# Kernel optimization log

Measured on AMD Instinct MI355X. Metric: run time of the kernel, lower is better.

## Reference

```python
import jax, jax.numpy as jnp
import numpy as np

N = 8192   # number of nodes
C = 16     # number of classes / clusters


def setup_inputs() -> dict:
    key = jax.random.key(0)
    k1, k2 = jax.random.split(key)
    H_i = jax.random.normal(k1, (N, C), dtype=jnp.float32)
    A_i = jax.random.normal(k2, (N, N), dtype=jnp.float32)
    return {"H_i": H_i, "A_i": A_i}


def reference(H_i, A_i):
    # adj = (A_i > 0), boolean adjacency (non-differentiable threshold)
    adj = (A_i > 0).astype(H_i.dtype)          # [N, N]
    deg = jnp.sum(adj, axis=0)                 # [N] node degrees
    s = jnp.sum(adj)                           # scalar: total edge weight (2m)
    # trace(H^T B H) with B = adj - outer(deg, deg)/s, computed without
    # materializing B:  trace(H^T adj H) = sum(H * (adj @ H)),
    # trace(H^T outer(deg,deg) H) = (deg @ H) . (deg @ H)
    quad = jnp.sum(H_i * (adj @ H_i))          # sum_c h_c^T adj h_c
    dH = deg @ H_i                             # [C]
    loss = (quad - jnp.dot(dH, dH) / s) / s
    return loss
```

## Files before the change

### kernel.cpp

```cpp
#include <hip/hip_runtime.h>
#include <hip/hip_bf16.h>
#include <stdint.h>

#define NN 8192
#define CC 16
#define RPB 64
#define COLSPLIT 16
#define CPB (NN / COLSPLIT)
#define NCHUNK (NN / 32)
#define ITERS (CPB / 32)
#define NBLK ((NN / RPB) * COLSPLIT)

typedef __attribute__((ext_vector_type(8))) short bf16x8;
typedef __attribute__((ext_vector_type(4))) float f32x4;
typedef __attribute__((ext_vector_type(4))) unsigned int u32x4;


__device__ __forceinline__ unsigned short f32_to_bf16(float f) {
  unsigned int u = __float_as_uint(f);
  u = u + 0x7FFFu + ((u >> 16) & 1u);
  return (unsigned short)(u >> 16);
}
__device__ __forceinline__ float bf16_to_f32(unsigned short h) {
  return __uint_as_float(((unsigned int)h) << 16);
}

__global__ void prep_btab(const float* __restrict__ H, u32x4* __restrict__ btab) {
  int t = blockIdx.x * blockDim.x + threadIdx.x;
  int lane = t & 63;
  int chunk = (t >> 6) & (NCHUNK - 1);
  int pass = t >> 14;
  int c = lane & 15, q = lane >> 4;
  int j0 = chunk * 32 + q * 8;
  unsigned int w[4];
#pragma unroll
  for (int p = 0; p < 4; ++p) {
    unsigned int r = 0;
#pragma unroll
    for (int e = 0; e < 2; ++e) {
      float x = H[(size_t)(j0 + 2 * p + e) * CC + c];
      unsigned short hb = f32_to_bf16(x);
      unsigned short bits = hb;
      if (pass) bits = f32_to_bf16(x - bf16_to_f32(hb));
      r |= ((unsigned int)bits) << (16 * e);
    }
    w[p] = r;
  }
  u32x4 o; o.x = w[0]; o.y = w[1]; o.z = w[2]; o.w = w[3];
  btab[t] = o;
}

__global__ __launch_bounds__(256, 4) void main_k(
    const float* __restrict__ A, const float* __restrict__ H,
    const u32x4* __restrict__ btab,
    double* __restrict__ quad_p, int* __restrict__ cnt_p,
    double* __restrict__ dh_p) {
  __shared__ float sdH[4][16];
  __shared__ float squad[4];
  __shared__ int scnt[4];

  int tid = threadIdx.x;
  int wave = tid >> 6, lane = tid & 63;
  int rb = blockIdx.x / COLSPLIT, cb = blockIdx.x % COLSPLIT;
  int m = lane & 15, q = lane >> 4;
  int row0 = rb * RPB + wave * 16;
  int col0 = cb * CPB;

  const float* arow = A + (size_t)(row0 + m) * NN + col0 + q * 8;
  int chunk0 = col0 >> 5;
  const u32x4* bth = btab + (size_t)chunk0 * 64 + lane;
  const u32x4* btl = bth + (size_t)NCHUNK * 64;

  f32x4 acc_h = {0.f, 0.f, 0.f, 0.f};
  f32x4 acc_l = {0.f, 0.f, 0.f, 0.f};
  int cnt = 0;

#pragma unroll 2
  for (int it = 0; it < ITERS; ++it) {
    f32x4 a0 = *(const f32x4*)(arow + it * 32);
    f32x4 a1 = *(const f32x4*)(arow + it * 32 + 4);
    u32x4 bh = bth[it * 64];
    u32x4 bl = btl[it * 64];
    unsigned int p0 = (a0.x > 0.f ? 0x3F80u : 0u) | (a0.y > 0.f ? 0x3F800000u : 0u);
    unsigned int p1 = (a0.z > 0.f ? 0x3F80u : 0u) | (a0.w > 0.f ? 0x3F800000u : 0u);
    unsigned int p2 = (a1.x > 0.f ? 0x3F80u : 0u) | (a1.y > 0.f ? 0x3F800000u : 0u);
    unsigned int p3 = (a1.z > 0.f ? 0x3F80u : 0u) | (a1.w > 0.f ? 0x3F800000u : 0u);
    cnt += __popc(p0 & 0x00800080u) + __popc(p1 & 0x00800080u) +
           __popc(p2 & 0x00800080u) + __popc(p3 & 0x00800080u);
    u32x4 af; af.x = p0; af.y = p1; af.z = p2; af.w = p3;
    bf16x8 afrag = __builtin_bit_cast(bf16x8, af);
    acc_h = __builtin_amdgcn_mfma_f32_16x16x32_bf16(afrag, __builtin_bit_cast(bf16x8, bh), acc_h, 0, 0, 0);
    acc_l = __builtin_amdgcn_mfma_f32_16x16x32_bf16(afrag, __builtin_bit_cast(bf16x8, bl), acc_l, 0, 0, 0);
  }

  f32x4 af = acc_h + acc_l;

  float rowsum = af.x + af.y + af.z + af.w;
  rowsum += __shfl_xor(rowsum, 16, 64);
  rowsum += __shfl_xor(rowsum, 32, 64);

  const float* hr = H + (size_t)(row0 + q * 4) * CC + m;
  float qp = af.x * hr[0] + af.y * hr[CC] + af.z * hr[2 * CC] + af.w * hr[3 * CC];
#pragma unroll
  for (int d = 1; d < 64; d <<= 1) qp += __shfl_xor(qp, d, 64);
#pragma unroll
  for (int d = 1; d < 64; d <<= 1) cnt += __shfl_xor(cnt, d, 64);

  if (lane < 16) sdH[wave][lane] = rowsum;
  if (lane == 0) { squad[wave] = qp; scnt[wave] = cnt; }
  __syncthreads();
  int bid = blockIdx.x;
  if (tid < 16) {
    dh_p[(size_t)bid * 16 + tid] =
        (double)(sdH[0][tid] + sdH[1][tid] + sdH[2][tid] + sdH[3][tid]);
  } else if (tid == 16) {
    quad_p[bid] = (double)(squad[0] + squad[1] + squad[2] + squad[3]);
  } else if (tid == 17) {
    cnt_p[bid] = scnt[0] + scnt[1] + scnt[2] + scnt[3];
  }
}

__global__ __launch_bounds__(256) void reduce_finalize(
    const double* __restrict__ quad_p, const int* __restrict__ cnt_p,
    const double* __restrict__ dh_p, float* __restrict__ out) {
  __shared__ double sq[4];
  __shared__ long long sc[4];
  __shared__ double sdh[4][16];
  int t = threadIdx.x;
  int wave = t >> 6, lane = t & 63;

  double q = 0.0;
  long long c = 0;
  double dh[16];
#pragma unroll
  for (int k = 0; k < 16; ++k) dh[k] = 0.0;

  for (int b = t; b < NBLK; b += 256) {
    q += quad_p[b];
    c += (long long)cnt_p[b];
#pragma unroll
    for (int k = 0; k < 16; ++k) dh[k] += dh_p[(size_t)b * 16 + k];
  }
#pragma unroll
  for (int d = 1; d < 64; d <<= 1) {
    q += __shfl_xor(q, d, 64);
    c += __shfl_xor(c, d, 64);
#pragma unroll
    for (int k = 0; k < 16; ++k) dh[k] += __shfl_xor(dh[k], d, 64);
  }
  if (lane == 0) {
    sq[wave] = q; sc[wave] = c;
#pragma unroll
    for (int k = 0; k < 16; ++k) sdh[wave][k] = dh[k];
  }
  __syncthreads();
  if (t == 0) {
    double Q = sq[0] + sq[1] + sq[2] + sq[3];
    double S = (double)(sc[0] + sc[1] + sc[2] + sc[3]);
    double D2 = 0.0;
#pragma unroll
    for (int k = 0; k < 16; ++k) {
      double v = sdh[0][k] + sdh[1][k] + sdh[2][k] + sdh[3][k];
      D2 += v * v;
    }
    out[0] = (float)((Q - D2 / S) / S);
  }
}

extern "C" void kernel_launch(void* const* d_in, const int* in_sizes, int n_in,
                              void* d_out, int out_size, void* d_ws, size_t ws_size,
                              hipStream_t stream) {
  const float* H = (const float*)d_in[0];
  const float* A = (const float*)d_in[1];
  if (n_in >= 2 && in_sizes[0] != NN * CC) {
    H = (const float*)d_in[1];
    A = (const float*)d_in[0];
  }
  float* out = (float*)d_out;
  char* ws = (char*)d_ws;
  u32x4* btab = (u32x4*)(ws + 8192);
  double* quad_p = (double*)(ws + (1 << 20));
  int* cnt_p = (int*)(ws + (1 << 20) + (32 << 10));
  double* dh_p = (double*)(ws + (1 << 20) + (64 << 10));

  prep_btab<<<(2 * NCHUNK * 64) / 256, 256, 0, stream>>>(H, btab);
  main_k<<<NBLK, 256, 0, stream>>>(A, H, btab, quad_p, cnt_p, dh_p);
  reduce_finalize<<<1, 256, 0, stream>>>(quad_p, cnt_p, dh_p, out);
}
```

Baseline: 373.6 us.

## Stage A tiles into LDS with async global_load_lds double buffering

```diff
diff --git a/kernel.cpp b/kernel.cpp
--- a/kernel.cpp
+++ b/kernel.cpp
@@ -8,8 +8,14 @@
 #define COLSPLIT 16
 #define CPB (NN / COLSPLIT)
 #define NCHUNK (NN / 32)
-#define ITERS (CPB / 32)
 #define NBLK ((NN / RPB) * COLSPLIT)
+
+#define TILE_C 64
+#define NT (CPB / TILE_C)
+#define UNIT_B 1040
+#define BUF_B (4 * UNIT_B)
+#define WAVE_B (2 * BUF_B)
+#define SMEM_B (4 * WAVE_B)
 
 typedef __attribute__((ext_vector_type(8))) short bf16x8;
 typedef __attribute__((ext_vector_type(4))) float f32x4;
@@ -23,6 +29,12 @@
 }
 __device__ __forceinline__ float bf16_to_f32(unsigned short h) {
   return __uint_as_float(((unsigned int)h) << 16);
+}
+
+__device__ __forceinline__ void stage16(const float* g, char* l) {
+  __builtin_amdgcn_global_load_lds(
+      (const __attribute__((address_space(1))) void*)g,
+      (__attribute__((address_space(3))) void*)l, 16, 0, 0);
 }
 
 __global__ void prep_btab(const float* __restrict__ H, u32x4* __restrict__ btab) {
@@ -55,6 +67,7 @@
     const u32x4* __restrict__ btab,
     double* __restrict__ quad_p, int* __restrict__ cnt_p,
     double* __restrict__ dh_p) {
+  __shared__ char smem[SMEM_B];
   __shared__ float sdH[4][16];
   __shared__ float squad[4];
   __shared__ int scnt[4];
@@ -65,9 +78,15 @@
   int m = lane & 15, q = lane >> 4;
   int row0 = rb * RPB + wave * 16;
   int col0 = cb * CPB;
-
-  const float* arow = A + (size_t)(row0 + m) * NN + col0 + q * 8;
   int chunk0 = col0 >> 5;
+
+  const float* gbase =
+      A + (size_t)(row0 + (lane >> 4)) * NN + col0 + (lane & 15) * 4;
+  char* lwave = smem + wave * WAVE_B;
+
+  const char* fbase =
+      lwave + (m >> 2) * UNIT_B + (m & 3) * 256 + q * 32;
+
   const u32x4* bth = btab + (size_t)chunk0 * 64 + lane;
   const u32x4* btl = bth + (size_t)NCHUNK * 64;
 
@@ -75,22 +94,42 @@
   f32x4 acc_l = {0.f, 0.f, 0.f, 0.f};
   int cnt = 0;
 
-#pragma unroll 2
-  for (int it = 0; it < ITERS; ++it) {
-    f32x4 a0 = *(const f32x4*)(arow + it * 32);
-    f32x4 a1 = *(const f32x4*)(arow + it * 32 + 4);
-    u32x4 bh = bth[it * 64];
-    u32x4 bl = btl[it * 64];
-    unsigned int p0 = (a0.x > 0.f ? 0x3F80u : 0u) | (a0.y > 0.f ? 0x3F800000u : 0u);
-    unsigned int p1 = (a0.z > 0.f ? 0x3F80u : 0u) | (a0.w > 0.f ? 0x3F800000u : 0u);
-    unsigned int p2 = (a1.x > 0.f ? 0x3F80u : 0u) | (a1.y > 0.f ? 0x3F800000u : 0u);
-    unsigned int p3 = (a1.z > 0.f ? 0x3F80u : 0u) | (a1.w > 0.f ? 0x3F800000u : 0u);
-    cnt += __popc(p0 & 0x00800080u) + __popc(p1 & 0x00800080u) +
-           __popc(p2 & 0x00800080u) + __popc(p3 & 0x00800080u);
-    u32x4 af; af.x = p0; af.y = p1; af.z = p2; af.w = p3;
-    bf16x8 afrag = __builtin_bit_cast(bf16x8, af);
-    acc_h = __builtin_amdgcn_mfma_f32_16x16x32_bf16(afrag, __builtin_bit_cast(bf16x8, bh), acc_h, 0, 0, 0);
-    acc_l = __builtin_amdgcn_mfma_f32_16x16x32_bf16(afrag, __builtin_bit_cast(bf16x8, bl), acc_l, 0, 0, 0);
+#pragma unroll
+  for (int u = 0; u < 4; ++u)
+    stage16(gbase + (size_t)(4 * u) * NN, lwave + u * UNIT_B);
+
+  for (int t = 0; t < NT; ++t) {
+    int b = t & 1;
+    if (t + 1 < NT) {
+#pragma unroll
+      for (int u = 0; u < 4; ++u)
+        stage16(gbase + (size_t)(4 * u) * NN + (t + 1) * TILE_C,
+                lwave + (b ^ 1) * BUF_B + u * UNIT_B);
+      asm volatile("s_waitcnt vmcnt(4)" ::: "memory");
+    } else {
+      asm volatile("s_waitcnt vmcnt(0)" ::: "memory");
+    }
+
+#pragma unroll
+    for (int kk = 0; kk < 2; ++kk) {
+      u32x4 bh = bth[(size_t)(t * 2 + kk) * 64];
+      u32x4 bl = btl[(size_t)(t * 2 + kk) * 64];
+      const f32x4* ap = (const f32x4*)(fbase + b * BUF_B + kk * 128);
+      f32x4 a0 = ap[0];
+      f32x4 a1 = ap[1];
+      unsigned int p0 = (a0.x > 0.f ? 0x3F80u : 0u) | (a0.y > 0.f ? 0x3F800000u : 0u);
+      unsigned int p1 = (a0.z > 0.f ? 0x3F80u : 0u) | (a0.w > 0.f ? 0x3F800000u : 0u);
+      unsigned int p2 = (a1.x > 0.f ? 0x3F80u : 0u) | (a1.y > 0.f ? 0x3F800000u : 0u);
+      unsigned int p3 = (a1.z > 0.f ? 0x3F80u : 0u) | (a1.w > 0.f ? 0x3F800000u : 0u);
+      cnt += __popc(p0 & 0x00800080u) + __popc(p1 & 0x00800080u) +
+             __popc(p2 & 0x00800080u) + __popc(p3 & 0x00800080u);
+      u32x4 af; af.x = p0; af.y = p1; af.z = p2; af.w = p3;
+      bf16x8 afrag = __builtin_bit_cast(bf16x8, af);
+      acc_h = __builtin_amdgcn_mfma_f32_16x16x32_bf16(
+          afrag, __builtin_bit_cast(bf16x8, bh), acc_h, 0, 0, 0);
+      acc_l = __builtin_amdgcn_mfma_f32_16x16x32_bf16(
+          afrag, __builtin_bit_cast(bf16x8, bl), acc_l, 0, 0, 0);
+    }
   }
 
   f32x4 af = acc_h + acc_l;
```

Measured after the change: 376.4 us. Within noise of the previous version (+0.8%).
